# Kernel optimization log

Hardware: AMD Instinct MI355X
Metric: run time of the kernel (lower is better)

Reference implementation:

```python
import jax, jax.numpy as jnp
import numpy as np

T, I, H, O = 8192, 64, 2048, 128


def setup_inputs() -> dict:
    key = jax.random.key(0)
    ks = jax.random.split(key, 8)
    s_ih = 1.0 / np.sqrt(H)
    return {
        "input_seq": jax.random.normal(ks[0], (T, I), dtype=jnp.float32),
        "W_ih": jax.random.uniform(ks[1], (4 * H, I), jnp.float32, -s_ih, s_ih),
        "W_hh": jax.random.uniform(ks[2], (4 * H, H), jnp.float32, -s_ih, s_ih),
        "b_ih": jax.random.uniform(ks[3], (4 * H,), jnp.float32, -s_ih, s_ih),
        "b_hh": jax.random.uniform(ks[4], (4 * H,), jnp.float32, -s_ih, s_ih),
        "W_lin": jax.random.uniform(ks[5], (O, H), jnp.float32, -s_ih, s_ih),
        "b_lin": jax.random.uniform(ks[6], (O,), jnp.float32, -s_ih, s_ih),
    }


def reference(input_seq, W_ih, W_hh, b_ih, b_hh, W_lin, b_lin):
    # Precompute input contributions for all timesteps: [T, 4H]
    x_gates = input_seq @ W_ih.T + b_ih + b_hh

    def cell(carry, xg):
        h, c = carry
        gates = xg + h @ W_hh.T  # [4H]
        i, f, g, o = jnp.split(gates, 4)
        i = jax.nn.sigmoid(i)
        f = jax.nn.sigmoid(f)
        g = jnp.tanh(g)
        o = jax.nn.sigmoid(o)
        c = f * c + i * g
        h = o * jnp.tanh(c)
        return (h, c), None

    h0 = jnp.zeros((H,), dtype=input_seq.dtype)
    c0 = jnp.zeros((H,), dtype=input_seq.dtype)
    (h_T, _), _ = jax.lax.scan(cell, (h0, c0), x_gates)
    # predictions[-1] == linear(out[-1]) since the Linear is per-timestep
    return h_T @ W_lin.T + b_lin
```

## Files before the change

### kernel.cpp

```cpp
#include <hip/hip_runtime.h>
#include <math.h>

#define T_STEPS 8192
#define I_DIM   64
#define H_DIM   2048
#define O_DIM   128
#define NBLK    256
#define NTHR    512
#define NSLOT   4
#define NAN_BITS 0x7FC00000u

typedef float v4f __attribute__((ext_vector_type(4)));

__device__ __forceinline__ float sigmoid_f(float x) {
    return 1.0f / (1.0f + __expf(-x));
}
__device__ __forceinline__ float tanh_fast(float x) {
    return 2.0f / (1.0f + __expf(-2.0f * x)) - 1.0f;
}

template <int CTRL>
__device__ __forceinline__ float dpp_add(float v) {
    int s = __builtin_amdgcn_update_dpp(0, __builtin_bit_cast(int, v),
                                        CTRL, 0xF, 0xF, true);
    return v + __builtin_bit_cast(float, s);
}
__device__ __forceinline__ float wave_sum64_lane63(float v) {
    v = dpp_add<0x111>(v);
    v = dpp_add<0x112>(v);
    v = dpp_add<0x114>(v);
    v = dpp_add<0x118>(v);
    v = dpp_add<0x142>(v);
    v = dpp_add<0x143>(v);
    return v;
}

__global__ void init_ws_kernel(unsigned int* Hbits) {
    int tid = blockIdx.x * blockDim.x + threadIdx.x;
    if (tid < NSLOT * H_DIM) {
        Hbits[tid] = (tid < H_DIM) ? 0u : NAN_BITS;
    }
}

__global__ __launch_bounds__(NTHR, 2) void lstm_persistent(
    const float* __restrict__ x,
    const float* __restrict__ Wih,
    const float* __restrict__ Whh,
    const float* __restrict__ bih,
    const float* __restrict__ bhh,
    unsigned int* __restrict__ Hbits)
{
    const int cu   = blockIdx.x;
    const int tid  = threadIdx.x;
    const int w    = tid >> 6;
    const int lane = tid & 63;

    __shared__ float hbuf[H_DIM];
    __shared__ float xbuf[I_DIM];
    __shared__ float gbuf[32];

    const int q    = w >> 1;
    const int joff = (w & 1) * 4;
    const int row0 = q * H_DIM + cu * 8 + joff;

    v4f wreg[4][8];
#pragma unroll
    for (int i = 0; i < 4; i++) {
        const float* p = Whh + (size_t)(row0 + i) * H_DIM + lane * 4;
#pragma unroll
        for (int m = 0; m < 8; m++)
            wreg[i][m] = *(const v4f*)(p + m * 256);
    }
    float xw[4];
    {
        const int xr = row0 + (lane >> 4);
        const float* p = Wih + (size_t)xr * I_DIM + (lane & 15) * 4;
#pragma unroll
        for (int m = 0; m < 4; m++) xw[m] = p[m];
    }
    float bias[4] = {0.f, 0.f, 0.f, 0.f};
    if (lane < 8) {
#pragma unroll
        for (int g = 0; g < 4; g++) {
            int r = g * H_DIM + cu * 8 + lane;
            bias[g] = bih[r] + bhh[r];
        }
    }
    float cstate = 0.0f;

    for (int t = 0; t < T_STEPS; t++) {
        const int slot_r = t & (NSLOT - 1);
        const int slot_w = (t + 1) & (NSLOT - 1);
        const int slot_z = (t + 2) & (NSLOT - 1);

        float xv_own = (tid < I_DIM) ? x[(size_t)t * I_DIM + tid] : 0.0f;

        {
            const unsigned int* Hr = Hbits + slot_r * H_DIM;
            unsigned int u0, u1, u2, u3;
            for (;;) {
                u0 = __hip_atomic_load(Hr + tid,             __ATOMIC_RELAXED, __HIP_MEMORY_SCOPE_AGENT);
                u1 = __hip_atomic_load(Hr + tid + 1 * NTHR,  __ATOMIC_RELAXED, __HIP_MEMORY_SCOPE_AGENT);
                u2 = __hip_atomic_load(Hr + tid + 2 * NTHR,  __ATOMIC_RELAXED, __HIP_MEMORY_SCOPE_AGENT);
                u3 = __hip_atomic_load(Hr + tid + 3 * NTHR,  __ATOMIC_RELAXED, __HIP_MEMORY_SCOPE_AGENT);
                bool miss = (u0 == NAN_BITS) | (u1 == NAN_BITS) |
                            (u2 == NAN_BITS) | (u3 == NAN_BITS);
                if (!miss) break;
                __builtin_amdgcn_s_sleep(2);
            }
            hbuf[tid]            = __uint_as_float(u0);
            hbuf[tid + 1 * NTHR] = __uint_as_float(u1);
            hbuf[tid + 2 * NTHR] = __uint_as_float(u2);
            hbuf[tid + 3 * NTHR] = __uint_as_float(u3);
            if (tid < I_DIM) xbuf[tid] = xv_own;
        }
        if (w == 0 && lane < 8) {
            __hip_atomic_store(Hbits + slot_z * H_DIM + cu * 8 + lane, NAN_BITS,
                               __ATOMIC_RELAXED, __HIP_MEMORY_SCOPE_AGENT);
        }
        __syncthreads();

        v4f av0 = {0.f,0.f,0.f,0.f}, av1 = {0.f,0.f,0.f,0.f};
        v4f av2 = {0.f,0.f,0.f,0.f}, av3 = {0.f,0.f,0.f,0.f};
#pragma unroll
        for (int m = 0; m < 8; m++) {
            v4f hv = *(const v4f*)&hbuf[m * 256 + lane * 4];
            av0 += wreg[0][m] * hv;
            av1 += wreg[1][m] * hv;
            av2 += wreg[2][m] * hv;
            av3 += wreg[3][m] * hv;
        }
        float acc0 = (av0[0] + av0[1]) + (av0[2] + av0[3]);
        float acc1 = (av1[0] + av1[1]) + (av1[2] + av1[3]);
        float acc2 = (av2[0] + av2[1]) + (av2[2] + av2[3]);
        float acc3 = (av3[0] + av3[1]) + (av3[2] + av3[3]);
        {
            float xp = 0.f;
            const int b = (lane & 15) * 4;
#pragma unroll
            for (int m = 0; m < 4; m++) xp += xw[m] * xbuf[b + m];
            const int sel = lane >> 4;
            acc0 += (sel == 0) ? xp : 0.0f;
            acc1 += (sel == 1) ? xp : 0.0f;
            acc2 += (sel == 2) ? xp : 0.0f;
            acc3 += (sel == 3) ? xp : 0.0f;
        }
        acc0 = wave_sum64_lane63(acc0);
        acc1 = wave_sum64_lane63(acc1);
        acc2 = wave_sum64_lane63(acc2);
        acc3 = wave_sum64_lane63(acc3);
        if (lane == 63) {
            gbuf[q * 8 + joff + 0] = acc0;
            gbuf[q * 8 + joff + 1] = acc1;
            gbuf[q * 8 + joff + 2] = acc2;
            gbuf[q * 8 + joff + 3] = acc3;
        }
        __syncthreads();

        if (lane < 8) {
            float gi = gbuf[0 * 8 + lane] + bias[0];
            float gf = gbuf[1 * 8 + lane] + bias[1];
            float gg = gbuf[2 * 8 + lane] + bias[2];
            float go = gbuf[3 * 8 + lane] + bias[3];
            float iv = sigmoid_f(gi);
            float fv = sigmoid_f(gf);
            float gv = tanh_fast(gg);
            float ov = sigmoid_f(go);
            cstate = fv * cstate + iv * gv;
            float hval = ov * tanh_fast(cstate);
            if (w == 0) {
                __hip_atomic_store(Hbits + slot_w * H_DIM + cu * 8 + lane,
                                   __float_as_uint(hval),
                                   __ATOMIC_RELAXED, __HIP_MEMORY_SCOPE_AGENT);
            }
        }
    }
}

__global__ void final_linear(const float* __restrict__ hT,
                             const float* __restrict__ Wlin,
                             const float* __restrict__ blin,
                             float* __restrict__ out)
{
    int gw   = (blockIdx.x * blockDim.x + threadIdx.x) >> 6;
    int lane = threadIdx.x & 63;
    if (gw < O_DIM) {
        const float* wp = Wlin + (size_t)gw * H_DIM;
        float s = 0.f;
        for (int k = lane; k < H_DIM; k += 64)
            s += wp[k] * hT[k];
#pragma unroll
        for (int off = 32; off; off >>= 1) s += __shfl_xor(s, off, 64);
        if (lane == 0) out[gw] = s + blin[gw];
    }
}

extern "C" void kernel_launch(void* const* d_in, const int* in_sizes, int n_in,
                              void* d_out, int out_size, void* d_ws, size_t ws_size,
                              hipStream_t stream)
{
    const float* x    = (const float*)d_in[0];
    const float* Wih  = (const float*)d_in[1];
    const float* Whh  = (const float*)d_in[2];
    const float* bih  = (const float*)d_in[3];
    const float* bhh  = (const float*)d_in[4];
    const float* Wlin = (const float*)d_in[5];
    const float* blin = (const float*)d_in[6];
    float* out = (float*)d_out;

    unsigned int* Hbits = (unsigned int*)d_ws;

    hipLaunchKernelGGL(init_ws_kernel, dim3((NSLOT * H_DIM + 255) / 256), dim3(256),
                       0, stream, Hbits);

    void* args[] = { (void*)&x, (void*)&Wih, (void*)&Whh, (void*)&bih, (void*)&bhh,
                     (void*)&Hbits };
    (void)hipLaunchCooperativeKernel(reinterpret_cast<void*>(lstm_persistent),
                                     dim3(NBLK), dim3(NTHR), args, 0, stream);

    hipLaunchKernelGGL(final_linear, dim3(32), dim3(256), 0, stream,
                       (const float*)Hbits, Wlin, blin, out);
}
```

Before: 19.20 ms.

## Replace second block barrier with LDS flag polling and vectorize hidden-state loads

Removes the second __syncthreads per timestep. Wave 0 now polls NaN-sentinel gate slots in shared memory instead of having all waves wait at a barrier, and it clears the slots after computing the cell update. The four scalar atomic loads of the hidden state become one dwordx4 inline-asm load with the sc1 cache bit, and the spin sleep is shortened. The aim is to cut per-step synchronization latency on the serial critical path. The cost is reliance on volatile LDS ordering, and a possible race if fast waves overwrite gate slots before they are cleared, although the first barrier at the next step probably prevents that.

```diff
diff --git a/kernel.cpp b/kernel.cpp
--- a/kernel.cpp
+++ b/kernel.cpp
@@ -10,7 +10,8 @@
 #define NSLOT   4
 #define NAN_BITS 0x7FC00000u
 
-typedef float v4f __attribute__((ext_vector_type(4)));
+typedef float        v4f __attribute__((ext_vector_type(4)));
+typedef unsigned int v4u __attribute__((ext_vector_type(4)));
 
 __device__ __forceinline__ float sigmoid_f(float x) {
     return 1.0f / (1.0f + __expf(-x));
@@ -57,7 +58,7 @@
 
     __shared__ float hbuf[H_DIM];
     __shared__ float xbuf[I_DIM];
-    __shared__ float gbuf[32];
+    __shared__ unsigned int gbits[32];
 
     const int q    = w >> 1;
     const int joff = (w & 1) * 4;
@@ -79,7 +80,7 @@
         for (int m = 0; m < 4; m++) xw[m] = p[m];
     }
     float bias[4] = {0.f, 0.f, 0.f, 0.f};
-    if (lane < 8) {
+    if (w == 0 && lane < 8) {
 #pragma unroll
         for (int g = 0; g < 4; g++) {
             int r = g * H_DIM + cu * 8 + lane;
@@ -87,6 +88,11 @@
         }
     }
     float cstate = 0.0f;
+
+    if (tid < 32) gbits[tid] = NAN_BITS;
+    __syncthreads();
+
+    volatile unsigned int* vg = gbits;
 
     for (int t = 0; t < T_STEPS; t++) {
         const int slot_r = t & (NSLOT - 1);
@@ -96,22 +102,19 @@
         float xv_own = (tid < I_DIM) ? x[(size_t)t * I_DIM + tid] : 0.0f;
 
         {
-            const unsigned int* Hr = Hbits + slot_r * H_DIM;
-            unsigned int u0, u1, u2, u3;
+            const unsigned int* Hr = Hbits + slot_r * H_DIM + tid * 4;
+            v4u u;
             for (;;) {
-                u0 = __hip_atomic_load(Hr + tid,             __ATOMIC_RELAXED, __HIP_MEMORY_SCOPE_AGENT);
-                u1 = __hip_atomic_load(Hr + tid + 1 * NTHR,  __ATOMIC_RELAXED, __HIP_MEMORY_SCOPE_AGENT);
-                u2 = __hip_atomic_load(Hr + tid + 2 * NTHR,  __ATOMIC_RELAXED, __HIP_MEMORY_SCOPE_AGENT);
-                u3 = __hip_atomic_load(Hr + tid + 3 * NTHR,  __ATOMIC_RELAXED, __HIP_MEMORY_SCOPE_AGENT);
-                bool miss = (u0 == NAN_BITS) | (u1 == NAN_BITS) |
-                            (u2 == NAN_BITS) | (u3 == NAN_BITS);
+                asm volatile(
+                    "global_load_dwordx4 %0, %1, off sc1\n\t"
+                    "s_waitcnt vmcnt(0)"
+                    : "=v"(u) : "v"(Hr) : "memory");
+                bool miss = (u[0] == NAN_BITS) | (u[1] == NAN_BITS) |
+                            (u[2] == NAN_BITS) | (u[3] == NAN_BITS);
                 if (!miss) break;
-                __builtin_amdgcn_s_sleep(2);
+                __builtin_amdgcn_s_sleep(1);
             }
-            hbuf[tid]            = __uint_as_float(u0);
-            hbuf[tid + 1 * NTHR] = __uint_as_float(u1);
-            hbuf[tid + 2 * NTHR] = __uint_as_float(u2);
-            hbuf[tid + 3 * NTHR] = __uint_as_float(u3);
+            *(v4u*)&hbuf[tid * 4] = u;
             if (tid < I_DIM) xbuf[tid] = xv_own;
         }
         if (w == 0 && lane < 8) {
@@ -150,29 +153,34 @@
         acc2 = wave_sum64_lane63(acc2);
         acc3 = wave_sum64_lane63(acc3);
         if (lane == 63) {
-            gbuf[q * 8 + joff + 0] = acc0;
-            gbuf[q * 8 + joff + 1] = acc1;
-            gbuf[q * 8 + joff + 2] = acc2;
-            gbuf[q * 8 + joff + 3] = acc3;
-        }
-        __syncthreads();
-
-        if (lane < 8) {
-            float gi = gbuf[0 * 8 + lane] + bias[0];
-            float gf = gbuf[1 * 8 + lane] + bias[1];
-            float gg = gbuf[2 * 8 + lane] + bias[2];
-            float go = gbuf[3 * 8 + lane] + bias[3];
-            float iv = sigmoid_f(gi);
-            float fv = sigmoid_f(gf);
-            float gv = tanh_fast(gg);
-            float ov = sigmoid_f(go);
+            vg[q * 8 + joff + 0] = __float_as_uint(acc0);
+            vg[q * 8 + joff + 1] = __float_as_uint(acc1);
+            vg[q * 8 + joff + 2] = __float_as_uint(acc2);
+            vg[q * 8 + joff + 3] = __float_as_uint(acc3);
+        }
+
+        if (w == 0 && lane < 8) {
+            unsigned int g0, g1, g2, g3;
+            do {
+                g0 = vg[0 * 8 + lane];
+                g1 = vg[1 * 8 + lane];
+                g2 = vg[2 * 8 + lane];
+                g3 = vg[3 * 8 + lane];
+            } while (__any((g0 == NAN_BITS) | (g1 == NAN_BITS) |
+                           (g2 == NAN_BITS) | (g3 == NAN_BITS)));
+            float iv = sigmoid_f(__uint_as_float(g0) + bias[0]);
+            float fv = sigmoid_f(__uint_as_float(g1) + bias[1]);
+            float gv = tanh_fast(__uint_as_float(g2) + bias[2]);
+            float ov = sigmoid_f(__uint_as_float(g3) + bias[3]);
             cstate = fv * cstate + iv * gv;
             float hval = ov * tanh_fast(cstate);
-            if (w == 0) {
-                __hip_atomic_store(Hbits + slot_w * H_DIM + cu * 8 + lane,
-                                   __float_as_uint(hval),
-                                   __ATOMIC_RELAXED, __HIP_MEMORY_SCOPE_AGENT);
-            }
+            __hip_atomic_store(Hbits + slot_w * H_DIM + cu * 8 + lane,
+                               __float_as_uint(hval),
+                               __ATOMIC_RELAXED, __HIP_MEMORY_SCOPE_AGENT);
+            vg[0 * 8 + lane] = NAN_BITS;
+            vg[1 * 8 + lane] = NAN_BITS;
+            vg[2 * 8 + lane] = NAN_BITS;
+            vg[3 * 8 + lane] = NAN_BITS;
         }
     }
 }
```

Measured after the change: 20.65 ms. 1.08x slower.
